# Kernel tuning notes

Measured on AMD Instinct MI355X. Metric: run time of the kernel, lower is better.

Reference implementation:

```python
import jax, jax.numpy as jnp
import numpy as np

C = 256        # out_ch / block dim
WS = 16        # window_size
HEADS = 4
HD = C // HEADS
MB = 128       # memory_blocks
LOW = C // 8   # down_rank = 8
SHIFTS = (0, 8, 0, 8)  # depth=4, shift_size = 0 if i%2==0 else 8
WF = 0.1       # weight_factor
EPS = 1e-5


def _rel_pos_index(ws):
    coords = np.stack(np.meshgrid(np.arange(ws), np.arange(ws), indexing="ij")).reshape(2, -1)
    rel = (coords[:, :, None] - coords[:, None, :]).transpose(1, 2, 0) + ws - 1
    return jnp.asarray(rel[..., 0] * (2 * ws - 1) + rel[..., 1])  # [N,N] int


def _shift_mask(H, W, ws, shift):
    # standard Swin shifted-window attention mask, computed statically
    img = np.zeros((H, W))
    cnt = 0
    sls = (slice(0, -ws), slice(-ws, -shift), slice(-shift, None))
    for hs in sls:
        for wss in sls:
            img[hs, wss] = cnt
            cnt += 1
    win = img.reshape(H // ws, ws, W // ws, ws).transpose(0, 2, 1, 3).reshape(-1, ws * ws)
    diff = win[:, None, :] - win[:, :, None]
    return jnp.asarray(np.where(diff != 0, -100.0, 0.0).astype(np.float32))  # [nW,N,N]


def _ln(x, g, b):
    mu = x.mean(-1, keepdims=True)
    var = ((x - mu) ** 2).mean(-1, keepdims=True)
    return (x - mu) * jax.lax.rsqrt(var + EPS) * g + b


def setup_inputs() -> dict:
    key = jax.random.key(0)
    ks = jax.random.split(key, 16)
    B, IN_CH, H, W, D = 8, 64, 64, 64, 4
    w = lambda k, shape: jax.random.normal(k, shape, jnp.float32) * 0.02
    return {
        "x": jax.random.normal(ks[0], (B, IN_CH, H, W), jnp.float32),
        "conv_w": w(ks[1], (C, IN_CH, 3, 3)),
        "bn_gamma": jnp.ones((C,), jnp.float32),
        "bn_beta": jnp.zeros((C,), jnp.float32),
        "bn_mean": jnp.zeros((C,), jnp.float32),
        "bn_var": jnp.ones((C,), jnp.float32),
        "ln1_g": jnp.ones((D, C), jnp.float32),
        "ln1_b": jnp.zeros((D, C), jnp.float32),
        "qkv_w": w(ks[2], (D, 3 * C, C)),
        "qkv_b": jnp.zeros((D, 3 * C), jnp.float32),
        "proj_w": w(ks[3], (D, C, C)),
        "proj_b": jnp.zeros((D, C), jnp.float32),
        "rpb": w(ks[4], (D, (2 * WS - 1) ** 2, HEADS)),
        "mem_bank": w(ks[5], (D, MB, LOW)),
        "down_w": w(ks[6], (D, LOW, C)),
        "down_b": jnp.zeros((D, LOW), jnp.float32),
        "up_w": w(ks[7], (D, C, LOW)),
        "up_b": jnp.zeros((D, C), jnp.float32),
        "ln2_g": jnp.ones((D, C), jnp.float32),
        "ln2_b": jnp.zeros((D, C), jnp.float32),
        "mlp_w1": w(ks[8], (D, 2 * C, C)),
        "mlp_b1": jnp.zeros((D, 2 * C), jnp.float32),
        "mlp_w2": w(ks[9], (D, C, 2 * C)),
        "mlp_b2": jnp.zeros((D, C), jnp.float32),
    }


def reference(x, conv_w, bn_gamma, bn_beta, bn_mean, bn_var, ln1_g, ln1_b,
              qkv_w, qkv_b, proj_w, proj_b, rpb, mem_bank, down_w, down_b,
              up_w, up_b, ln2_g, ln2_b, mlp_w1, mlp_b1, mlp_w2, mlp_b2):
    # conv 3x3 + BN (inference form) + ReLU stem
    y = jax.lax.conv_general_dilated(x, conv_w, (1, 1), ((1, 1), (1, 1)),
                                     dimension_numbers=("NCHW", "OIHW", "NCHW"))
    s = bn_gamma * jax.lax.rsqrt(bn_var + EPS)
    y = jax.nn.relu(y * s[None, :, None, None] + (bn_beta - bn_mean * s)[None, :, None, None])

    B, _, H, W = y.shape
    nH, nW_ = H // WS, W // WS
    nWin, N = nH * nW_, WS * WS
    rpi = _rel_pos_index(WS)
    t = jnp.transpose(y, (0, 2, 3, 1))  # [B,H,W,C]

    for i, shift in enumerate(SHIFTS):
        short = t
        z = _ln(t, ln1_g[i], ln1_b[i])
        if shift:
            z = jnp.roll(z, (-shift, -shift), axis=(1, 2))
        # window partition -> [B*nWin, N, C]
        win = z.reshape(B, nH, WS, nW_, WS, C).transpose(0, 1, 3, 2, 4, 5).reshape(B * nWin, N, C)
        qkv = win @ qkv_w[i].T + qkv_b[i]
        q, k, v = jnp.split(qkv, 3, axis=-1)
        q = q.reshape(-1, N, HEADS, HD).transpose(0, 2, 1, 3)
        k = k.reshape(-1, N, HEADS, HD).transpose(0, 2, 1, 3)
        v = v.reshape(-1, N, HEADS, HD).transpose(0, 2, 1, 3)
        attn = jnp.einsum("whnd,whmd->whnm", q, k) * (HD ** -0.5)
        attn = attn + rpb[i][rpi].transpose(2, 0, 1)[None]  # relative position bias
        if shift:
            mask = _shift_mask(H, W, WS, shift)  # [nWin,N,N]
            attn = (attn.reshape(B, nWin, HEADS, N, N) + mask[None, :, None]).reshape(B * nWin, HEADS, N, N)
        attn = jax.nn.softmax(attn, axis=-1)
        o = jnp.einsum("whnm,whmd->whnd", attn, v).transpose(0, 2, 1, 3).reshape(-1, N, C)
        # low-rank memory bank cross-attention (memory_blocks=128, down_rank=8)
        lowf = o @ down_w[i].T + down_b[i]                       # [B*nWin,N,LOW]
        a = jax.nn.softmax(lowf @ mem_bank[i].T, axis=-1)        # attend over 128 memory slots
        o = o + WF * ((a @ mem_bank[i]) @ up_w[i].T + up_b[i])
        o = o @ proj_w[i].T + proj_b[i]
        # window reverse
        z = o.reshape(B, nH, nW_, WS, WS, C).transpose(0, 1, 3, 2, 4, 5).reshape(B, H, W, C)
        if shift:
            z = jnp.roll(z, (shift, shift), axis=(1, 2))
        t = short + z  # drop_path is identity in deterministic/eval mode
        h = _ln(t, ln2_g[i], ln2_b[i])
        t = t + (jax.nn.gelu(h @ mlp_w1[i].T + mlp_b1[i]) @ mlp_w2[i].T + mlp_b2[i])
    return jnp.transpose(t, (0, 3, 1, 2))  # [B,C,H,W]
```

## Files before the change

### kernel.cpp

```cpp
#include <hip/hip_runtime.h>

using frag_ab = __attribute__((ext_vector_type(8))) short;
using f4v     = __attribute__((ext_vector_type(4))) float;
using u8v     = __attribute__((ext_vector_type(8))) unsigned short;
using u4v     = __attribute__((ext_vector_type(4))) unsigned short;

__device__ __forceinline__ float b2f(unsigned short u){
  return __uint_as_float(((unsigned int)u) << 16);
}
__device__ __forceinline__ unsigned short f2b(float f){
  unsigned int x = __float_as_uint(f);
  unsigned int r = x + 0x7fffu + ((x >> 16) & 1u);
  return (unsigned short)(r >> 16);
}
__device__ __forceinline__ float h2f(unsigned short u){
  _Float16 h; __builtin_memcpy(&h, &u, 2); return (float)h;
}
__device__ __forceinline__ unsigned short f2h(float f){
  _Float16 h = (_Float16)f; unsigned short u; __builtin_memcpy(&u, &h, 2); return u;
}
__device__ __forceinline__ float hexp2(float x){
#if __has_builtin(__builtin_amdgcn_exp2f)
  return __builtin_amdgcn_exp2f(x);
#else
  return exp2f(x);
#endif
}
__device__ __forceinline__ float hrcp(float x){
#if __has_builtin(__builtin_amdgcn_rcpf)
  return __builtin_amdgcn_rcpf(x);
#else
  return 1.0f / x;
#endif
}
__device__ __forceinline__ unsigned int cvtpk(float lo, float hi){
  unsigned int r;
  asm("v_cvt_pk_bf16_f32 %0, %1, %2" : "=v"(r) : "v"(lo), "v"(hi));
  return r;
}
__device__ __forceinline__ void gl16(const void* g, void* l){
  __builtin_amdgcn_global_load_lds(
      (const __attribute__((address_space(1))) unsigned int*)g,
      (__attribute__((address_space(3))) unsigned int*)l, 16, 0, 0);
}

#define MFMA_BF16 __builtin_amdgcn_mfma_f32_16x16x32_bf16

static constexpr size_t OFF_T   = 0;
static constexpr size_t OFF_R1  = 33554432ull;
static constexpr size_t OFF_V   = OFF_R1 + 37748736ull;
static constexpr size_t OFF_VT  = OFF_V + 16777216ull;
static constexpr size_t OFF_ZH  = OFF_VT + 16777216ull;
static constexpr size_t OFF_A   = OFF_ZH + 16777216ull;
static constexpr size_t OFF_WB  = OFF_A + 8388608ull;
static constexpr size_t WB_CONVW = 0;
static constexpr size_t WB_QKVW  = 294912;
static constexpr size_t WB_PROJW = 1867776;
static constexpr size_t WB_MLP1W = 2392064;
static constexpr size_t WB_MLP2W = 3440640;
static constexpr size_t WB_W1    = 4489216;
static constexpr size_t WB_W2T   = 4751360;
static constexpr size_t WB_BLOG  = 5013504;
static constexpr size_t WB_CS    = 5015552;
static constexpr size_t WB_CSH   = 5016576;
static constexpr size_t WB_BIASP = 5017600;
static constexpr size_t WB_PW2   = WB_BIASP + 5242880;
static constexpr size_t WB_PB2   = WB_PW2 + 786432;

__global__ __launch_bounds__(256) void prep_k(
    const float* __restrict__ conv_w, const float* __restrict__ bn_g, const float* __restrict__ bn_b,
    const float* __restrict__ bn_m, const float* __restrict__ bn_v,
    const float* __restrict__ qkv_w, const float* __restrict__ proj_w,
    const float* __restrict__ mlp_w1, const float* __restrict__ mlp_w2,
    const float* __restrict__ mem_b, const float* __restrict__ down_w, const float* __restrict__ down_b,
    const float* __restrict__ up_w, const float* __restrict__ rpb,
    unsigned short* convwb, unsigned short* qkvwb, unsigned short* projwb,
    unsigned short* mlp1wb, unsigned short* mlp2wb, unsigned short* W1b, unsigned short* W2Tb,
    unsigned short* biasPb, float* blogf, float* convS, float* convSh)
{
  int idx = blockIdx.x * 256 + threadIdx.x;
  if (idx < 256){
    float s = bn_g[idx] * rsqrtf(bn_v[idx] + 1e-5f);
    convS[idx] = s; convSh[idx] = bn_b[idx] - bn_m[idx] * s; return;
  }
  idx -= 256;
  if (idx < 147456){
    int co = idx / 576, kk = idx % 576;
    int t9 = kk >> 6, ci = kk & 63, ky = t9 / 3, kx = t9 % 3;
    convwb[idx] = f2b(conv_w[((co*64 + ci)*3 + ky)*3 + kx]); return;
  }
  idx -= 147456;
  if (idx < 786432){ qkvwb[idx] = f2b(qkv_w[idx]); return; }
  idx -= 786432;
  if (idx < 262144){ projwb[idx] = f2b(proj_w[idx]); return; }
  idx -= 262144;
  if (idx < 524288){ mlp1wb[idx] = f2b(mlp_w1[idx]); return; }
  idx -= 524288;
  if (idx < 524288){ mlp2wb[idx] = f2b(mlp_w2[idx]); return; }
  idx -= 524288;
  if (idx < 131072){
    int i = idx >> 15, rem = idx & 32767, s = rem >> 8, c = rem & 255;
    float acc = 0.f;
    for (int j = 0; j < 32; ++j) acc += mem_b[(i*128 + s)*32 + j] * down_w[(i*32 + j)*256 + c];
    W1b[idx] = f2b(acc * 1.44269504f); return;
  }
  idx -= 131072;
  if (idx < 131072){
    int i = idx >> 15, rem = idx & 32767, c = rem >> 7, s = rem & 127;
    float acc = 0.f;
    for (int j = 0; j < 32; ++j) acc += mem_b[(i*128 + s)*32 + j] * up_w[(i*256 + c)*32 + j];
    W2Tb[idx] = f2b(acc); return;
  }
  idx -= 131072;
  if (idx < 512){
    int i = idx >> 7, s = idx & 127;
    float acc = 0.f;
    for (int j = 0; j < 32; ++j) acc += mem_b[(i*128 + s)*32 + j] * down_b[i*32 + j];
    blogf[idx] = acc * 1.44269504f; return;
  }
  idx -= 512;
  if (idx < 2621440){
    int t = idx >> 18, h = (idx >> 16) & 3, rest = idx & 65535;
    int qb = rest >> 12, kb = (rest >> 8) & 15, q15 = (rest >> 4) & 15, cm = rest & 15;
    int layer, var;
    if (t == 0){ layer = 0; var = 0; }
    else if (t <= 4){ layer = 1; var = t - 1; }
    else if (t == 5){ layer = 2; var = 0; }
    else { layer = 3; var = t - 6; }
    int ri = (qb - kb + 15)*31 + (q15 - cm + 15);
    float b = rpb[((size_t)layer*961 + ri)*4 + h];
    bool mk = ((var & 2) && ((qb < 8) != (kb < 8))) || ((var & 1) && ((q15 < 8) != (cm < 8)));
    if (mk) b -= 100.0f;
    biasPb[idx] = f2b(b * 1.44269504f);
  }
}

__global__ __launch_bounds__(256) void prep2_k(const float* __restrict__ proj_w,
    const float* __restrict__ up_b, const float* __restrict__ proj_b,
    const unsigned short* __restrict__ W2Tb, unsigned short* __restrict__ pw2, float* __restrict__ pb2)
{
  int idx = blockIdx.x * 256 + threadIdx.x;
  if (idx < 1024){
    int i = idx >> 8, o = idx & 255;
    float acc = proj_b[i*256 + o];
    for (int c = 0; c < 256; ++c) acc += 0.1f * up_b[i*256 + c] * proj_w[((size_t)(i*256 + o))*256 + c];
    pb2[idx] = acc; return;
  }
  idx -= 1024;
  if (idx < 262144){
    int i = idx >> 16, rem = idx & 65535, o = rem >> 8, c = rem & 255;
    pw2[((size_t)(i*256 + o))*384 + c] = f2b(proj_w[((size_t)(i*256 + o))*256 + c]); return;
  }
  idx -= 262144;
  if (idx < 131072){
    int i = idx >> 15, rem = idx & 32767, o = rem >> 7, s = rem & 127;
    float acc = 0.f;
    for (int c = 0; c < 256; ++c)
      acc += proj_w[((size_t)(i*256 + o))*256 + c] * b2f(W2Tb[(i*256 + c)*128 + s]);
    pw2[((size_t)(i*256 + o))*384 + 256 + s] = f2b(0.1f * acc);
  }
}

__global__ __launch_bounds__(256) void pad_k(const float* __restrict__ x, unsigned short* __restrict__ xp)
{
  const int bid = blockIdx.x;
  const int b = bid / 66, hp = bid % 66;
  const int tid = threadIdx.x;
  unsigned short* orow = xp + ((size_t)(b*66 + hp))*66*64;
  const u8v Z8 = {0,0,0,0,0,0,0,0};
  if (hp == 0 || hp == 65){
    for (int s = tid; s < 528; s += 256) *(u8v*)&orow[s*8] = Z8;
    return;
  }
  __shared__ float ls[64][65];
  const int h = hp - 1;
  {
    int cc = tid >> 2, w4 = (tid & 3)*16;
    const float* src = &x[((size_t)(b*64 + cc)*64 + h)*64 + w4];
    #pragma unroll
    for (int j = 0; j < 4; ++j){
      float4 v = *(const float4*)&src[j*4];
      ls[w4 + j*4 + 0][cc] = v.x; ls[w4 + j*4 + 1][cc] = v.y;
      ls[w4 + j*4 + 2][cc] = v.z; ls[w4 + j*4 + 3][cc] = v.w;
    }
  }
  __syncthreads();
  if (tid < 16){
    int wp = (tid >> 3) * 65;
    *(u8v*)&orow[(size_t)wp*64 + (tid & 7)*8] = Z8;
  }
  int w = tid >> 2, c0 = (tid & 3)*16;
  u8v o0, o1;
  #pragma unroll
  for (int e = 0; e < 8; ++e){ o0[e] = f2b(ls[w][c0+e]); o1[e] = f2b(ls[w][c0+8+e]); }
  *(u8v*)&orow[(size_t)(w+1)*64 + c0] = o0;
  *(u8v*)&orow[(size_t)(w+1)*64 + c0 + 8] = o1;
}

struct Ep {
  const float* c0; const float* c1;
  const float* lg; const float* lb;
  unsigned short* t; float* outp;
  unsigned short* o0; unsigned short* o2;
  unsigned short* q; unsigned short* k; unsigned short* v;
  const unsigned short* in0;
  int shift;
};
enum { M_CONV=0, M_QKV=1, M_MEM1S=2, M_PROJLN=3, M_MLP1=4, M_MLP2LN=5, M_MLP2OUT=6 };

template<int MODE, int TM, int TN, int KC, int NT, int GX>
__global__ __launch_bounds__(NT) void g512_k(const unsigned short* __restrict__ X,
                                             const unsigned short* __restrict__ W, Ep ep)
{
  __shared__ __align__(16) unsigned short Als[2][TM*32];
  __shared__ __align__(16) unsigned short Bls[2][TN*32];
  const int tid = threadIdx.x, wid = tid >> 6, lane = tid & 63, g = lane >> 4, l15 = lane & 15;
  constexpr int NW = TN/64;
  const int wr = wid / NW, wc = wid % NW;
  const int row0 = (GX ? blockIdx.y : blockIdx.x) * TM;
  const int col0 = (GX ? blockIdx.x : blockIdx.y) * TN;
  constexpr int KT = KC >> 5;
  constexpr int NA = (TM*4)/NT, NB = (TN*4)/NT;

  const unsigned short* gA[NA]; const unsigned short* gA2[NA]; int rbA[NA];
  #pragma unroll
  for (int i = 0; i < NA; ++i){
    int s = tid + NT*i, r = s >> 2, p = s & 3, lb = p ^ ((r >> 1) & 3);
    gA2[i] = nullptr;
    if constexpr (MODE == M_CONV){
      int ar = row0 + r, bi = ar >> 12, h = (ar >> 6) & 63, w = ar & 63;
      rbA[i] = ((bi*66 + h + 1)*66 + (w + 1))*64 + lb*8; gA[i] = nullptr;
    } else {
      constexpr int KA = (MODE == M_PROJLN) ? 256 : KC;
      gA[i] = &X[(size_t)(row0 + r)*KA + lb*8]; rbA[i] = 0;
      if constexpr (MODE == M_PROJLN) gA2[i] = &ep.in0[(size_t)(row0 + r)*128 + lb*8];
    }
  }
  const unsigned short* gB[NB];
  #pragma unroll
  for (int i = 0; i < NB; ++i){
    int s = tid + NT*i, r = s >> 2, p = s & 3, lb = p ^ ((r >> 1) & 3);
    gB[i] = &W[(size_t)(col0 + r)*KC + lb*8];
  }

  f4v acc[4][4] = {};

  auto stage = [&](int kt, int buf){
    #pragma unroll
    for (int i = 0; i < NA; ++i){
      if constexpr (MODE == M_CONV){
        int t9 = kt >> 1, ky = t9 / 3, kx = t9 - ky*3;
        int koff = ((ky - 1)*66 + (kx - 1))*64 + (kt & 1)*32;
        gl16(X + rbA[i] + koff, &Als[buf][(tid + NT*i)*8]);
      } else if constexpr (MODE == M_PROJLN){
        if (kt < 8) gl16(gA[i] + kt*32, &Als[buf][(tid + NT*i)*8]);
        else        gl16(gA2[i] + (kt - 8)*32, &Als[buf][(tid + NT*i)*8]);
      } else {
        gl16(gA[i] + kt*32, &Als[buf][(tid + NT*i)*8]);
      }
    }
    #pragma unroll
    for (int i = 0; i < NB; ++i) gl16(gB[i] + kt*32, &Bls[buf][(tid + NT*i)*8]);
  };
  auto compute = [&](const unsigned short* A, const unsigned short* B){
    frag_ab af[4], bv[4];
    #pragma unroll
    for (int a = 0; a < 4; ++a){ int r = wr*64 + a*16 + l15; int pb = g ^ ((r >> 1) & 3);
      af[a] = *(const frag_ab*)&A[r*32 + pb*8]; }
    #pragma unroll
    for (int b = 0; b < 4; ++b){ int r = wc*64 + b*16 + l15; int pb = g ^ ((r >> 1) & 3);
      bv[b] = *(const frag_ab*)&B[r*32 + pb*8]; }
    #pragma unroll
    for (int a = 0; a < 4; ++a)
      #pragma unroll
      for (int b = 0; b < 4; ++b)
        acc[a][b] = MFMA_BF16(af[a], bv[b], acc[a][b], 0, 0, 0);
  };

  stage(0, 0);
  __syncthreads();
  for (int kt = 0; kt < KT; kt += 2){
    stage(kt + 1, 1);
    compute(Als[0], Bls[0]);
    __syncthreads();
    if (kt + 2 < KT) stage(kt + 2, 0);
    compute(Als[1], Bls[1]);
    __syncthreads();
  }

  float* red = (float*)&Als[0][0];

  if constexpr (MODE == M_QKV){
    const int which = col0 >> 8;
    #pragma unroll
    for (int a = 0; a < 4; ++a){
      #pragma unroll
      for (int b = 0; b < 4; ++b){
        const int grow0 = row0 + wr*64 + a*16 + g*4;
        const int hd = b*16 + l15;
        const float bv = ep.c0[col0 + wc*64 + hd];
        if (which == 2){
          int tok0 = grow0 & 255;
          int pos = (tok0 & ~31) | ((tok0 & 12) << 1) | ((tok0 & 16) >> 2);
          u4v o;
          #pragma unroll
          for (int r = 0; r < 4; ++r) o[r] = f2b(acc[a][b][r] + bv);
          *(u4v*)&ep.v[(((size_t)((grow0 >> 8)*4 + wc)*64 + hd)*256) + pos] = o;
        } else {
          unsigned short* dst = (which == 0) ? ep.q : ep.k;
          float sc = (which == 0) ? 0.18033688f : 1.0f;
          #pragma unroll
          for (int r = 0; r < 4; ++r){
            int grow = grow0 + r;
            dst[(((size_t)(grow >> 8)*4 + wc)*256 + (grow & 255))*64 + hd] = f2b((acc[a][b][r] + bv) * sc);
          }
        }
      }
    }
  } else if constexpr (MODE == M_MEM1S){
    #pragma unroll
    for (int a = 0; a < 4; ++a){
      #pragma unroll
      for (int r = 0; r < 4; ++r){
        float s1 = 0.f;
        #pragma unroll
        for (int b = 0; b < 4; ++b){
          int bcol = wc*64 + b*16 + l15;
          float e = hexp2(acc[a][b][r] + ep.c0[bcol]);
          acc[a][b][r] = e; s1 += e;
        }
        s1 += __shfl_xor(s1, 1); s1 += __shfl_xor(s1, 2);
        s1 += __shfl_xor(s1, 4); s1 += __shfl_xor(s1, 8);
        if (l15 == 0){
          int rl = wr*64 + a*16 + g*4 + r;
          red[rl*NW + wc] = s1;
        }
      }
    }
    __syncthreads();
    #pragma unroll
    for (int a = 0; a < 4; ++a){
      #pragma unroll
      for (int r = 0; r < 4; ++r){
        int rl = wr*64 + a*16 + g*4 + r;
        float inv = 1.0f / (red[rl*NW] + red[rl*NW + 1]);
        int grow = row0 + rl;
        #pragma unroll
        for (int b = 0; b < 4; ++b){
          int bcol = wc*64 + b*16 + l15;
          ep.o0[(size_t)grow*128 + bcol] = f2b(acc[a][b][r] * inv);
        }
      }
    }
  } else if constexpr (MODE == M_MLP1){
    #pragma unroll
    for (int a = 0; a < 4; ++a)
      #pragma unroll
      for (int b = 0; b < 4; ++b)
        #pragma unroll
        for (int r = 0; r < 4; ++r){
          int grow = row0 + wr*64 + a*16 + g*4 + r;
          int gcol = col0 + wc*64 + b*16 + l15;
          float xq = acc[a][b][r] + ep.c0[gcol];
          float x3 = xq*xq*xq;
          float e = hexp2(xq*2.3022115f + x3*0.10294856f);
          float gl = xq - xq*hrcp(e + 1.0f);
          ep.o0[(size_t)grow*512 + gcol] = f2b(gl);
        }
  } else if constexpr (MODE == M_MLP2OUT){
    #pragma unroll
    for (int a = 0; a < 4; ++a){
      #pragma unroll
      for (int b = 0; b < 4; ++b){
        const int grow0 = row0 + wr*64 + a*16 + g*4;
        const int bcol = wc*64 + b*16 + l15;
        float4 vv;
        #pragma unroll
        for (int r = 0; r < 4; ++r)
          (&vv.x)[r] = h2f(ep.t[(size_t)(grow0 + r)*256 + bcol]) + acc[a][b][r] + ep.c0[bcol];
        *(float4*)&ep.outp[((size_t)((grow0 >> 12)*256 + bcol))*4096 + (grow0 & 4095)] = vv;
      }
    }
  } else {
    #pragma unroll
    for (int a = 0; a < 4; ++a){
      #pragma unroll
      for (int r = 0; r < 4; ++r){
        const int grow = row0 + wr*64 + a*16 + g*4 + r;
        int srow;
        if constexpr (MODE == M_PROJLN){
          int win = grow >> 8, tok = grow & 255;
          int bb = win >> 4, whh = (win >> 2) & 3, www = win & 3, rr = tok >> 4, cc = tok & 15;
          srow = (bb*64 + ((whh*16 + rr + ep.shift) & 63))*64 + ((www*16 + cc + ep.shift) & 63);
        } else srow = grow;
        float s1 = 0.f, s2 = 0.f;
        #pragma unroll
        for (int b = 0; b < 4; ++b){
          int bcol = wc*64 + b*16 + l15;
          float v = acc[a][b][r];
          if constexpr (MODE == M_CONV) v = fmaxf(v*ep.c0[bcol] + ep.c1[bcol], 0.f);
          else v = h2f(ep.t[(size_t)srow*256 + bcol]) + v + ep.c0[bcol];
          acc[a][b][r] = v;
          ep.t[(size_t)srow*256 + bcol] = f2h(v);
          s1 += v; s2 += v*v;
        }
        s1 += __shfl_xor(s1, 1); s2 += __shfl_xor(s2, 1);
        s1 += __shfl_xor(s1, 2); s2 += __shfl_xor(s2, 2);
        s1 += __shfl_xor(s1, 4); s2 += __shfl_xor(s2, 4);
        s1 += __shfl_xor(s1, 8); s2 += __shfl_xor(s2, 8);
        if (l15 == 0){
          int rl = wr*64 + a*16 + g*4 + r;
          red[rl*8 + wc*2]     = s1;
          red[rl*8 + wc*2 + 1] = s2;
        }
      }
    }
    __syncthreads();
    #pragma unroll
    for (int a = 0; a < 4; ++a){
      #pragma unroll
      for (int r = 0; r < 4; ++r){
        const int grow = row0 + wr*64 + a*16 + g*4 + r;
        int rl = wr*64 + a*16 + g*4 + r;
        float s1 = red[rl*8] + red[rl*8+2] + red[rl*8+4] + red[rl*8+6];
        float s2 = red[rl*8+1] + red[rl*8+3] + red[rl*8+5] + red[rl*8+7];
        float mu = s1 * (1.0f/256.0f);
        float var = s2 * (1.0f/256.0f) - mu*mu;
        float rstd = rsqrtf(var + 1e-5f);
        unsigned short* zo = (MODE == M_MLP2LN) ? ep.o2 : ep.o0;
        int drow;
        if constexpr (MODE == M_PROJLN){
          int win = grow >> 8, tok = grow & 255;
          int bb = win >> 4, whh = (win >> 2) & 3, www = win & 3, rr = tok >> 4, cc = tok & 15;
          drow = (bb*64 + ((whh*16 + rr + ep.shift) & 63))*64 + ((www*16 + cc + ep.shift) & 63);
        } else {
          int bb2 = grow >> 12, h = (grow >> 6) & 63, w = grow & 63;
          int hs = (h - ep.shift) & 63, ws = (w - ep.shift) & 63;
          drow = (bb2*16 + (hs >> 4)*4 + (ws >> 4))*256 + (hs & 15)*16 + (ws & 15);
        }
        #pragma unroll
        for (int b = 0; b < 4; ++b){
          int bcol = wc*64 + b*16 + l15;
          float v = acc[a][b][r];
          zo[(size_t)drow*256 + bcol] = f2b((v - mu)*rstd*ep.lg[bcol] + ep.lb[bcol]);
        }
      }
    }
  }
}

__global__ __launch_bounds__(512, 4) void attn_k(const unsigned short* __restrict__ qg_,
    const unsigned short* __restrict__ kg_, const unsigned short* __restrict__ vt_,
    const unsigned short* __restrict__ biasP, unsigned short* __restrict__ ob, int shift)
{
  __shared__ __align__(16) unsigned short Kl[16384];
  __shared__ __align__(16) unsigned short Vl[16384];
  const int tid = threadIdx.x, wid = tid >> 6, lane = tid & 63, g = lane >> 4, q15 = lane & 15;
  const int blk = blockIdx.x, win = blk >> 2, head = blk & 3;
  const int wh = (win >> 2) & 3, ww = win & 3;
  const unsigned short* kg = kg_ + (size_t)blk*16384;
  const unsigned short* vg = vt_ + (size_t)blk*16384;
  const unsigned short* qg = qg_ + (size_t)blk*16384;
  const int var = shift ? (((wh == 3) ? 2 : 0) | ((ww == 3) ? 1 : 0)) : 0;
  const unsigned short* bT = biasP + ((size_t)var*4 + head)*65536;

  #pragma unroll
  for (int it = 0; it < 4; ++it){
    int s = it*512 + tid;
    int r = s >> 3, lb = (s & 7) ^ (r & 7);
    gl16(&kg[r*64 + lb*8], &Kl[s*8]);
    int hd = s >> 5, cc = s & 31, cs = (cc & 16) | ((cc & 15) ^ (hd & 15));
    gl16(&vg[hd*256 + cs*8], &Vl[s*8]);
  }
  __syncthreads();

  const f4v Z4 = {0.f, 0.f, 0.f, 0.f};
  for (int c = 0; c < 2; ++c){
    const int nq = wid*32 + c*16 + q15;
    const int qb = wid*2 + c;
    frag_ab qf0 = *(const frag_ab*)&qg[nq*64 + g*8];
    frag_ab qf1 = *(const frag_ab*)&qg[nq*64 + 32 + g*8];
    unsigned int pk[32];
    float vsum = 0.f;
    #pragma unroll
    for (int t2 = 0; t2 < 16; ++t2){
      int r = t2*16 + q15;
      f4v a = Z4;
      { int pb = g ^ (r & 7);
        frag_ab ak = *(const frag_ab*)&Kl[r*64 + pb*8];
        a = MFMA_BF16(ak, qf0, a, 0, 0, 0); }
      { int pb = (4 + g) ^ (r & 7);
        frag_ab ak = *(const frag_ab*)&Kl[r*64 + pb*8];
        a = MFMA_BF16(ak, qf1, a, 0, 0, 0); }
      u4v bb = *(const u4v*)&bT[((qb*16 + t2)*16 + q15)*16 + g*4];
      float p0 = hexp2(a[0] + b2f(bb[0]));
      float p1 = hexp2(a[1] + b2f(bb[1]));
      float p2 = hexp2(a[2] + b2f(bb[2]));
      float p3 = hexp2(a[3] + b2f(bb[3]));
      vsum += (p0 + p1) + (p2 + p3);
      pk[2*t2]   = cvtpk(p0, p1);
      pk[2*t2+1] = cvtpk(p2, p3);
    }
    vsum += __shfl_xor(vsum, 16);
    vsum += __shfl_xor(vsum, 32);
    float inv = 1.0f / vsum;
    float invl[4];
    #pragma unroll
    for (int r = 0; r < 4; ++r) invl[r] = __shfl(inv, g*4 + r);
    f4v oc[4];
    #pragma unroll
    for (int nn = 0; nn < 4; ++nn) oc[nn] = Z4;
    __builtin_amdgcn_s_setprio(1);
    #pragma unroll
    for (int s = 0; s < 8; ++s){
      union { frag_ab f; unsigned int u[4]; } pa;
      pa.u[0] = pk[4*s + 0];
      pa.u[1] = pk[4*s + 1];
      pa.u[2] = pk[4*s + 2];
      pa.u[3] = pk[4*s + 3];
      #pragma unroll
      for (int nn = 0; nn < 4; ++nn){
        int hd = nn*16 + q15;
        int cc = s*4 + g;
        int cs = (cc & 16) | ((cc & 15) ^ (hd & 15));
        frag_ab bv = *(const frag_ab*)&Vl[hd*256 + cs*8];
        oc[nn] = MFMA_BF16(pa.f, bv, oc[nn], 0, 0, 0);
      }
    }
    __builtin_amdgcn_s_setprio(0);
    #pragma unroll
    for (int nn = 0; nn < 4; ++nn)
      #pragma unroll
      for (int r = 0; r < 4; ++r){
        int qq = wid*32 + c*16 + g*4 + r;
        ob[((size_t)(win*256 + qq))*256 + head*64 + nn*16 + q15] = f2b(oc[nn][r] * invl[r]);
      }
  }
}

extern "C" void kernel_launch(void* const* d_in, const int* in_sizes, int n_in,
                              void* d_out, int out_size, void* d_ws, size_t ws_size,
                              hipStream_t stream)
{
  (void)in_sizes; (void)n_in; (void)out_size; (void)ws_size;
  const float* x      = (const float*)d_in[0];
  const float* conv_w = (const float*)d_in[1];
  const float* bn_g   = (const float*)d_in[2];
  const float* bn_b   = (const float*)d_in[3];
  const float* bn_m   = (const float*)d_in[4];
  const float* bn_v   = (const float*)d_in[5];
  const float* ln1_g  = (const float*)d_in[6];
  const float* ln1_b  = (const float*)d_in[7];
  const float* qkv_w  = (const float*)d_in[8];
  const float* qkv_b  = (const float*)d_in[9];
  const float* proj_w = (const float*)d_in[10];
  const float* proj_b = (const float*)d_in[11];
  const float* rpb    = (const float*)d_in[12];
  const float* mem_b  = (const float*)d_in[13];
  const float* down_w = (const float*)d_in[14];
  const float* down_b = (const float*)d_in[15];
  const float* up_w   = (const float*)d_in[16];
  const float* up_b   = (const float*)d_in[17];
  const float* ln2_g  = (const float*)d_in[18];
  const float* ln2_b  = (const float*)d_in[19];
  const float* mlp_w1 = (const float*)d_in[20];
  const float* mlp_b1 = (const float*)d_in[21];
  const float* mlp_w2 = (const float*)d_in[22];
  const float* mlp_b2 = (const float*)d_in[23];

  char* ws = (char*)d_ws;
  unsigned short* tbuf  = (unsigned short*)(ws + OFF_T);
  unsigned short* xpb   = (unsigned short*)(ws + OFF_R1);
  unsigned short* qbuf  = (unsigned short*)(ws + OFF_R1);
  unsigned short* kbuf  = (unsigned short*)(ws + OFF_R1 + 16777216ull);
  unsigned short* gbuf  = (unsigned short*)(ws + OFF_R1);
  unsigned short* hbuf  = (unsigned short*)(ws + OFF_V);
  unsigned short* vtbuf = (unsigned short*)(ws + OFF_VT);
  unsigned short* zbuf  = (unsigned short*)(ws + OFF_ZH);
  unsigned short* abuf  = (unsigned short*)(ws + OFF_A);
  unsigned short* convwb = (unsigned short*)(ws + OFF_WB + WB_CONVW);
  unsigned short* qkvwb  = (unsigned short*)(ws + OFF_WB + WB_QKVW);
  unsigned short* projwb = (unsigned short*)(ws + OFF_WB + WB_PROJW);
  unsigned short* mlp1wb = (unsigned short*)(ws + OFF_WB + WB_MLP1W);
  unsigned short* mlp2wb = (unsigned short*)(ws + OFF_WB + WB_MLP2W);
  unsigned short* W1b    = (unsigned short*)(ws + OFF_WB + WB_W1);
  unsigned short* W2Tb   = (unsigned short*)(ws + OFF_WB + WB_W2T);
  float*          blogf  = (float*)(ws + OFF_WB + WB_BLOG);
  float*          convS  = (float*)(ws + OFF_WB + WB_CS);
  float*          convSh = (float*)(ws + OFF_WB + WB_CSH);
  unsigned short* biasPb = (unsigned short*)(ws + OFF_WB + WB_BIASP);
  unsigned short* pw2b   = (unsigned short*)(ws + OFF_WB + WB_PW2);
  float*          pb2f   = (float*)(ws + OFF_WB + WB_PB2);

  prep_k<<<20036, 256, 0, stream>>>(conv_w, bn_g, bn_b, bn_m, bn_v, qkv_w, proj_w, mlp_w1, mlp_w2,
                                    mem_b, down_w, down_b, up_w, rpb,
                                    convwb, qkvwb, projwb, mlp1wb, mlp2wb, W1b, W2Tb, biasPb,
                                    blogf, convS, convSh);
  prep2_k<<<1540, 256, 0, stream>>>(proj_w, up_b, proj_b, W2Tb, pw2b, pb2f);
  pad_k<<<528, 256, 0, stream>>>(x, xpb);
  { Ep ep{convS, convSh, ln1_g, ln1_b, tbuf, nullptr, zbuf, nullptr, nullptr, nullptr, nullptr, nullptr, 0};
    g512_k<M_CONV,64,256,576,256,0><<<dim3(512,1), 256, 0, stream>>>(xpb, convwb, ep); }

  static const int tb[4] = {0, 1, 5, 6};
  for (int i = 0; i < 4; ++i){
    int shift = (i & 1) ? 8 : 0;
    int shift_next = ((i + 1) & 1) ? 8 : 0;
    { Ep ep{qkv_b + i*768, nullptr, nullptr, nullptr, nullptr, nullptr, nullptr, nullptr, qbuf, kbuf, vtbuf, nullptr, 0};
      g512_k<M_QKV,64,256,256,256,1><<<dim3(3,512), 256, 0, stream>>>(zbuf, qkvwb + (size_t)i*196608, ep); }
    attn_k<<<512, 512, 0, stream>>>(qbuf, kbuf, vtbuf, biasPb + (size_t)tb[i]*262144, zbuf, shift);
    { Ep ep{blogf + i*128, nullptr, nullptr, nullptr, nullptr, nullptr, abuf, nullptr, nullptr, nullptr, nullptr, nullptr, 0};
      g512_k<M_MEM1S,128,128,256,256,0><<<dim3(256,1), 256, 0, stream>>>(zbuf, W1b + (size_t)i*32768, ep); }
    { Ep ep{pb2f + i*256, nullptr, ln2_g + i*256, ln2_b + i*256, tbuf, nullptr, hbuf, nullptr, nullptr, nullptr, nullptr, abuf, shift};
      g512_k<M_PROJLN,64,256,384,256,0><<<dim3(512,1), 256, 0, stream>>>(zbuf, pw2b + (size_t)i*98304, ep); }
    { Ep ep{mlp_b1 + i*512, nullptr, nullptr, nullptr, nullptr, nullptr, gbuf, nullptr, nullptr, nullptr, nullptr, nullptr, 0};
      g512_k<M_MLP1,64,256,256,256,1><<<dim3(2,512), 256, 0, stream>>>(hbuf, mlp1wb + (size_t)i*131072, ep); }
    if (i < 3){
      Ep ep{mlp_b2 + i*256, nullptr, ln1_g + (i+1)*256, ln1_b + (i+1)*256, tbuf, nullptr, nullptr, zbuf, nullptr, nullptr, nullptr, nullptr, shift_next};
      g512_k<M_MLP2LN,64,256,512,256,0><<<dim3(512,1), 256, 0, stream>>>(gbuf, mlp2wb + (size_t)i*131072, ep);
    } else {
      Ep ep{mlp_b2 + i*256, nullptr, nullptr, nullptr, tbuf, (float*)d_out, nullptr, nullptr, nullptr, nullptr, nullptr, nullptr, 0};
      g512_k<M_MLP2OUT,64,256,512,256,0><<<dim3(512,1), 256, 0, stream>>>(gbuf, mlp2wb + (size_t)i*131072, ep);
    }
  }
}
```

Measured before the change: 611.0 us.

## Fuse projection+LayerNorm GEMM with MLP1 GEMM, keeping LN output in LDS

Adds a projmlp_k kernel that runs the projection GEMM (with the memory-bank term and residual add), then LayerNorm, and writes the normalized rows into shared memory. The same block then runs the first MLP GEMM with GELU directly from that LDS tile. This removes the intermediate hbuf round-trip through global memory and one kernel launch per layer. In exchange each block uses about 72KB of LDS and processes all 512 MLP1 columns serially, so occupancy and grid parallelism go down compared with the separate 2x512 MLP1 grid.

Result: slower. 718.7 us (+17.6%).

```diff
diff --git a/kernel.cpp b/kernel.cpp
--- a/kernel.cpp
+++ b/kernel.cpp
@@ -206,7 +206,7 @@
   const unsigned short* in0;
   int shift;
 };
-enum { M_CONV=0, M_QKV=1, M_MEM1S=2, M_PROJLN=3, M_MLP1=4, M_MLP2LN=5, M_MLP2OUT=6 };
+enum { M_CONV=0, M_QKV=1, M_MEM1S=2, M_MLP2LN=5, M_MLP2OUT=6 };
 
 template<int MODE, int TM, int TN, int KC, int NT, int GX>
 __global__ __launch_bounds__(NT) void g512_k(const unsigned short* __restrict__ X,
@@ -222,18 +222,15 @@
   constexpr int KT = KC >> 5;
   constexpr int NA = (TM*4)/NT, NB = (TN*4)/NT;
 
-  const unsigned short* gA[NA]; const unsigned short* gA2[NA]; int rbA[NA];
+  const unsigned short* gA[NA]; int rbA[NA];
   #pragma unroll
   for (int i = 0; i < NA; ++i){
     int s = tid + NT*i, r = s >> 2, p = s & 3, lb = p ^ ((r >> 1) & 3);
-    gA2[i] = nullptr;
     if constexpr (MODE == M_CONV){
       int ar = row0 + r, bi = ar >> 12, h = (ar >> 6) & 63, w = ar & 63;
       rbA[i] = ((bi*66 + h + 1)*66 + (w + 1))*64 + lb*8; gA[i] = nullptr;
     } else {
-      constexpr int KA = (MODE == M_PROJLN) ? 256 : KC;
-      gA[i] = &X[(size_t)(row0 + r)*KA + lb*8]; rbA[i] = 0;
-      if constexpr (MODE == M_PROJLN) gA2[i] = &ep.in0[(size_t)(row0 + r)*128 + lb*8];
+      gA[i] = &X[(size_t)(row0 + r)*KC + lb*8]; rbA[i] = 0;
     }
   }
   const unsigned short* gB[NB];
@@ -252,9 +249,6 @@
         int t9 = kt >> 1, ky = t9 / 3, kx = t9 - ky*3;
         int koff = ((ky - 1)*66 + (kx - 1))*64 + (kt & 1)*32;
         gl16(X + rbA[i] + koff, &Als[buf][(tid + NT*i)*8]);
-      } else if constexpr (MODE == M_PROJLN){
-        if (kt < 8) gl16(gA[i] + kt*32, &Als[buf][(tid + NT*i)*8]);
-        else        gl16(gA2[i] + (kt - 8)*32, &Als[buf][(tid + NT*i)*8]);
       } else {
         gl16(gA[i] + kt*32, &Als[buf][(tid + NT*i)*8]);
       }
@@ -352,21 +346,6 @@
         }
       }
     }
-  } else if constexpr (MODE == M_MLP1){
-    #pragma unroll
-    for (int a = 0; a < 4; ++a)
-      #pragma unroll
-      for (int b = 0; b < 4; ++b)
-        #pragma unroll
-        for (int r = 0; r < 4; ++r){
-          int grow = row0 + wr*64 + a*16 + g*4 + r;
-          int gcol = col0 + wc*64 + b*16 + l15;
-          float xq = acc[a][b][r] + ep.c0[gcol];
-          float x3 = xq*xq*xq;
-          float e = hexp2(xq*2.3022115f + x3*0.10294856f);
-          float gl = xq - xq*hrcp(e + 1.0f);
-          ep.o0[(size_t)grow*512 + gcol] = f2b(gl);
-        }
   } else if constexpr (MODE == M_MLP2OUT){
     #pragma unroll
     for (int a = 0; a < 4; ++a){
@@ -387,21 +366,15 @@
       #pragma unroll
       for (int r = 0; r < 4; ++r){
         const int grow = row0 + wr*64 + a*16 + g*4 + r;
-        int srow;
-        if constexpr (MODE == M_PROJLN){
-          int win = grow >> 8, tok = grow & 255;
-          int bb = win >> 4, whh = (win >> 2) & 3, www = win & 3, rr = tok >> 4, cc = tok & 15;
-          srow = (bb*64 + ((whh*16 + rr + ep.shift) & 63))*64 + ((www*16 + cc + ep.shift) & 63);
-        } else srow = grow;
         float s1 = 0.f, s2 = 0.f;
         #pragma unroll
         for (int b = 0; b < 4; ++b){
           int bcol = wc*64 + b*16 + l15;
           float v = acc[a][b][r];
           if constexpr (MODE == M_CONV) v = fmaxf(v*ep.c0[bcol] + ep.c1[bcol], 0.f);
-          else v = h2f(ep.t[(size_t)srow*256 + bcol]) + v + ep.c0[bcol];
+          else v = h2f(ep.t[(size_t)grow*256 + bcol]) + v + ep.c0[bcol];
           acc[a][b][r] = v;
-          ep.t[(size_t)srow*256 + bcol] = f2h(v);
+          ep.t[(size_t)grow*256 + bcol] = f2h(v);
           s1 += v; s2 += v*v;
         }
         s1 += __shfl_xor(s1, 1); s2 += __shfl_xor(s2, 1);
@@ -428,21 +401,168 @@
         float var = s2 * (1.0f/256.0f) - mu*mu;
         float rstd = rsqrtf(var + 1e-5f);
         unsigned short* zo = (MODE == M_MLP2LN) ? ep.o2 : ep.o0;
-        int drow;
-        if constexpr (MODE == M_PROJLN){
-          int win = grow >> 8, tok = grow & 255;
-          int bb = win >> 4, whh = (win >> 2) & 3, www = win & 3, rr = tok >> 4, cc = tok & 15;
-          drow = (bb*64 + ((whh*16 + rr + ep.shift) & 63))*64 + ((www*16 + cc + ep.shift) & 63);
-        } else {
-          int bb2 = grow >> 12, h = (grow >> 6) & 63, w = grow & 63;
-          int hs = (h - ep.shift) & 63, ws = (w - ep.shift) & 63;
-          drow = (bb2*16 + (hs >> 4)*4 + (ws >> 4))*256 + (hs & 15)*16 + (ws & 15);
-        }
+        int bb2 = grow >> 12, h = (grow >> 6) & 63, w = grow & 63;
+        int hs = (h - ep.shift) & 63, ws = (w - ep.shift) & 63;
+        int drow = (bb2*16 + (hs >> 4)*4 + (ws >> 4))*256 + (hs & 15)*16 + (ws & 15);
         #pragma unroll
         for (int b = 0; b < 4; ++b){
           int bcol = wc*64 + b*16 + l15;
           float v = acc[a][b][r];
           zo[(size_t)drow*256 + bcol] = f2b((v - mu)*rstd*ep.lg[bcol] + ep.lb[bcol]);
+        }
+      }
+    }
+  }
+}
+
+__global__ __launch_bounds__(256) void projmlp_k(
+    const unsigned short* __restrict__ Z, const unsigned short* __restrict__ A2,
+    const unsigned short* __restrict__ PW2, const unsigned short* __restrict__ W1M,
+    const float* __restrict__ pb2, const float* __restrict__ lg2, const float* __restrict__ lb2,
+    const float* __restrict__ mb1, unsigned short* __restrict__ t, unsigned short* __restrict__ gout,
+    int shift)
+{
+  __shared__ __align__(16) unsigned short Als[2][2048];
+  __shared__ __align__(16) unsigned short Bls[2][8192];
+  __shared__ __align__(16) unsigned short hL[16384];
+  const int tid = threadIdx.x, wid = tid >> 6, lane = tid & 63, gq = lane >> 4, l15 = lane & 15;
+  const int wc = wid;
+  const int row0 = blockIdx.x * 64;
+
+  const int rA = tid >> 2, pA = tid & 3;
+  const int lbA = pA ^ ((rA >> 1) & 3);
+  const unsigned short* gAz = &Z[(size_t)(row0 + rA)*256 + lbA*8];
+  const unsigned short* gAa = &A2[(size_t)(row0 + rA)*128 + lbA*8];
+  const unsigned short* gB1[4];
+  const unsigned short* gB2[4];
+  #pragma unroll
+  for (int i = 0; i < 4; ++i){
+    int s = tid + 256*i, r = s >> 2, p = s & 3, lb = p ^ ((r >> 1) & 3);
+    gB1[i] = &PW2[(size_t)r*384 + lb*8];
+    gB2[i] = &W1M[(size_t)r*256 + lb*8];
+  }
+
+  f4v acc[4][4] = {};
+
+  auto stage1 = [&](int kt, int buf){
+    if (kt < 8) gl16(gAz + kt*32, &Als[buf][tid*8]);
+    else        gl16(gAa + (kt - 8)*32, &Als[buf][tid*8]);
+    #pragma unroll
+    for (int i = 0; i < 4; ++i) gl16(gB1[i] + kt*32, &Bls[buf][(tid + 256*i)*8]);
+  };
+  auto stage2 = [&](int cb, int kt, int buf){
+    #pragma unroll
+    for (int i = 0; i < 4; ++i) gl16(gB2[i] + (size_t)cb*65536 + kt*32, &Bls[buf][(tid + 256*i)*8]);
+  };
+  auto compute = [&](const unsigned short* A, const unsigned short* B){
+    frag_ab af[4], bv[4];
+    #pragma unroll
+    for (int a = 0; a < 4; ++a){ int r = a*16 + l15; int pb = gq ^ ((r >> 1) & 3);
+      af[a] = *(const frag_ab*)&A[r*32 + pb*8]; }
+    #pragma unroll
+    for (int b = 0; b < 4; ++b){ int r = wc*64 + b*16 + l15; int pb = gq ^ ((r >> 1) & 3);
+      bv[b] = *(const frag_ab*)&B[r*32 + pb*8]; }
+    #pragma unroll
+    for (int a = 0; a < 4; ++a)
+      #pragma unroll
+      for (int b = 0; b < 4; ++b)
+        acc[a][b] = MFMA_BF16(af[a], bv[b], acc[a][b], 0, 0, 0);
+  };
+
+  stage1(0, 0);
+  __syncthreads();
+  for (int kt = 0; kt < 12; kt += 2){
+    stage1(kt + 1, 1);
+    compute(Als[0], Bls[0]);
+    __syncthreads();
+    if (kt + 2 < 12) stage1(kt + 2, 0);
+    compute(Als[1], Bls[1]);
+    __syncthreads();
+  }
+
+  float* red = (float*)&Als[0][0];
+  #pragma unroll
+  for (int a = 0; a < 4; ++a){
+    #pragma unroll
+    for (int r = 0; r < 4; ++r){
+      const int grow = row0 + a*16 + gq*4 + r;
+      int win = grow >> 8, tok = grow & 255;
+      int bb = win >> 4, whh = (win >> 2) & 3, www = win & 3, rr = tok >> 4, cc = tok & 15;
+      int srow = (bb*64 + ((whh*16 + rr + shift) & 63))*64 + ((www*16 + cc + shift) & 63);
+      float s1 = 0.f, s2 = 0.f;
+      #pragma unroll
+      for (int b = 0; b < 4; ++b){
+        int bcol = wc*64 + b*16 + l15;
+        float v = h2f(t[(size_t)srow*256 + bcol]) + acc[a][b][r] + pb2[bcol];
+        acc[a][b][r] = v;
+        t[(size_t)srow*256 + bcol] = f2h(v);
+        s1 += v; s2 += v*v;
+      }
+      s1 += __shfl_xor(s1, 1); s2 += __shfl_xor(s2, 1);
+      s1 += __shfl_xor(s1, 2); s2 += __shfl_xor(s2, 2);
+      s1 += __shfl_xor(s1, 4); s2 += __shfl_xor(s2, 4);
+      s1 += __shfl_xor(s1, 8); s2 += __shfl_xor(s2, 8);
+      if (l15 == 0){
+        int rl = a*16 + gq*4 + r;
+        red[rl*8 + wc*2]     = s1;
+        red[rl*8 + wc*2 + 1] = s2;
+      }
+    }
+  }
+  __syncthreads();
+  #pragma unroll
+  for (int a = 0; a < 4; ++a){
+    #pragma unroll
+    for (int r = 0; r < 4; ++r){
+      int rl = a*16 + gq*4 + r;
+      float s1 = red[rl*8] + red[rl*8+2] + red[rl*8+4] + red[rl*8+6];
+      float s2 = red[rl*8+1] + red[rl*8+3] + red[rl*8+5] + red[rl*8+7];
+      float mu = s1 * (1.0f/256.0f);
+      float var = s2 * (1.0f/256.0f) - mu*mu;
+      float rstd = rsqrtf(var + 1e-5f);
+      #pragma unroll
+      for (int b = 0; b < 4; ++b){
+        int bcol = wc*64 + b*16 + l15;
+        float hv = (acc[a][b][r] - mu)*rstd*lg2[bcol] + lb2[bcol];
+        int ktc = bcol >> 5, pc = (bcol >> 3) & 3, ec = bcol & 7;
+        hL[ktc*2048 + rl*32 + ((pc ^ ((rl >> 1) & 3)))*8 + ec] = f2b(hv);
+      }
+    }
+  }
+  __syncthreads();
+
+  for (int cb = 0; cb < 2; ++cb){
+    #pragma unroll
+    for (int a = 0; a < 4; ++a)
+      #pragma unroll
+      for (int b = 0; b < 4; ++b)
+        acc[a][b] = f4v{0.f, 0.f, 0.f, 0.f};
+    stage2(cb, 0, 0);
+    __syncthreads();
+    for (int kt = 0; kt < 8; kt += 2){
+      stage2(cb, kt + 1, 1);
+      compute(&hL[kt*2048], Bls[0]);
+      __syncthreads();
+      if (kt + 2 < 8) stage2(cb, kt + 2, 0);
+      compute(&hL[(kt + 1)*2048], Bls[1]);
+      __syncthreads();
+    }
+    #pragma unroll
+    for (int a = 0; a < 4; ++a){
+      #pragma unroll
+      for (int r = 0; r < 4; ++r){
+        const int grow = row0 + a*16 + gq*4 + r;
+        int win = grow >> 8, tok = grow & 255;
+        int bb = win >> 4, whh = (win >> 2) & 3, www = win & 3, rr = tok >> 4, cc = tok & 15;
+        int srow = (bb*64 + ((whh*16 + rr + shift) & 63))*64 + ((www*16 + cc + shift) & 63);
+        #pragma unroll
+        for (int b = 0; b < 4; ++b){
+          int gcol = cb*256 + wc*64 + b*16 + l15;
+          float xq = acc[a][b][r] + mb1[gcol];
+          float x3 = xq*xq*xq;
+          float e = hexp2(xq*2.3022115f + x3*0.10294856f);
+          float gl = xq - xq*hrcp(e + 1.0f);
+          gout[(size_t)srow*512 + gcol] = f2b(gl);
         }
       }
     }
@@ -574,7 +694,6 @@
   unsigned short* qbuf  = (unsigned short*)(ws + OFF_R1);
   unsigned short* kbuf  = (unsigned short*)(ws + OFF_R1 + 16777216ull);
   unsigned short* gbuf  = (unsigned short*)(ws + OFF_R1);
-  unsigned short* hbuf  = (unsigned short*)(ws + OFF_V);
   unsigned short* vtbuf = (unsigned short*)(ws + OFF_VT);
   unsigned short* zbuf  = (unsigned short*)(ws + OFF_ZH);
   unsigned short* abuf  = (unsigned short*)(ws + OFF_A);
@@ -610,10 +729,9 @@
     attn_k<<<512, 512, 0, stream>>>(qbuf, kbuf, vtbuf, biasPb + (size_t)tb[i]*262144, zbuf, shift);
     { Ep ep{blogf + i*128, nullptr, nullptr, nullptr, nullptr, nullptr, abuf, nullptr, nullptr, nullptr, nullptr, nullptr, 0};
       g512_k<M_MEM1S,128,128,256,256,0><<<dim3(256,1), 256, 0, stream>>>(zbuf, W1b + (size_t)i*32768, ep); }
-    { Ep ep{pb2f + i*256, nullptr, ln2_g + i*256, ln2_b + i*256, tbuf, nullptr, hbuf, nullptr, nullptr, nullptr, nullptr, abuf, shift};
-      g512_k<M_PROJLN,64,256,384,256,0><<<dim3(512,1), 256, 0, stream>>>(zbuf, pw2b + (size_t)i*98304, ep); }
-    { Ep ep{mlp_b1 + i*512, nullptr, nullptr, nullptr, nullptr, nullptr, gbuf, nullptr, nullptr, nullptr, nullptr, nullptr, 0};
-      g512_k<M_MLP1,64,256,256,256,1><<<dim3(2,512), 256, 0, stream>>>(hbuf, mlp1wb + (size_t)i*131072, ep); }
+    projmlp_k<<<512, 256, 0, stream>>>(zbuf, abuf, pw2b + (size_t)i*98304, mlp1wb + (size_t)i*131072,
+                                       pb2f + i*256, ln2_g + i*256, ln2_b + i*256, mlp_b1 + i*512,
+                                       tbuf, gbuf, shift);
     if (i < 3){
       Ep ep{mlp_b2 + i*256, nullptr, ln1_g + (i+1)*256, ln1_b + (i+1)*256, tbuf, nullptr, nullptr, zbuf, nullptr, nullptr, nullptr, nullptr, shift_next};
       g512_k<M_MLP2LN,64,256,512,256,0><<<dim3(512,1), 256, 0, stream>>>(gbuf, mlp2wb + (size_t)i*131072, ep);
```
